# Optimization experiments

Hardware: AMD Instinct MI355X
Metric: run time of the kernel (lower is better)

Reference implementation:

```python
import jax, jax.numpy as jnp
import numpy as np

# Directional rectangle cumulative max: max over the axis-aligned rectangle
# between each pixel and one image corner.

def _rectmax(x, rev_h, rev_w):
    y = jax.lax.cummax(x, axis=2, reverse=rev_h)
    return jax.lax.cummax(y, axis=3, reverse=rev_w)


def _guided_pool(xq, gq, rev_h, rev_w):
    # Guided landmark pool: each pixel takes max of itself and the directional
    # cumulative max restricted to guide==1 positions. With guide == ones this
    # reduces to the plain directional rectangle cummax (the un-guided pool).
    neg = jnp.finfo(xq.dtype).min
    masked = jnp.where(gq > 0, xq, neg)
    return jnp.maximum(xq, _rectmax(masked, rev_h, rev_w))

# (rev_h, rev_w) for TopLeft, TopRight, BottomLeft, BottomRight pools
_DIRS = [(True, True), (True, False), (False, True), (False, False)]


def setup_inputs() -> dict:
    key = jax.random.key(0)
    k1, k2, k3 = jax.random.split(key, 3)
    B, C, H, W = 16, 256, 64, 64
    Cout, K = 256, 3
    x = jax.random.normal(k1, (B, C, H, W), jnp.float32)
    weight = jax.random.normal(k2, (Cout, C, K, K), jnp.float32) * 0.02
    bias = jax.random.normal(k3, (Cout,), jnp.float32) * 0.02
    return {"x": x, "weight": weight, "bias": bias}


def reference(x, weight, bias):
    B, C, H, W = x.shape
    Q = C // 4
    # Original torch code squares x IN PLACE via chunk() views before pooling.
    xsq = x * x
    # Per-quadrant channel energy and its global (row, col) argmax -> one-hot guide.
    energy = xsq.reshape(B, 4, Q, H, W).sum(axis=2)            # [B,4,H,W]
    idx = jnp.argmax(energy.reshape(B, 4, H * W), axis=-1)     # [B,4]
    onehot = (jnp.arange(H * W) == idx[..., None]).astype(x.dtype)
    guide = jnp.broadcast_to(onehot.reshape(B, 4, 1, H, W), (B, 4, Q, H, W)).reshape(B, C, H, W)
    # Four directional guided pools, one per channel quadrant, then conv.
    xs = jnp.split(xsq, 4, axis=1)
    gs = jnp.split(guide, 4, axis=1)
    pooled = jnp.concatenate(
        [_guided_pool(xs[i], gs[i], *_DIRS[i]) for i in range(4)], axis=1)
    out = jax.lax.conv_general_dilated(
        pooled, weight, window_strides=(1, 1), padding='SAME',
        dimension_numbers=('NCHW', 'OIHW', 'NCHW'))
    return out + bias[None, :, None, None]
```

## Files before the change

### kernel.cpp

```cpp
#include <hip/hip_runtime.h>
#include <cstddef>

#define B_   16
#define C_   256
#define HW_  4096

typedef __attribute__((ext_vector_type(8)))  short bf16x8;
typedef __attribute__((ext_vector_type(16))) float f32x16;

static __device__ __forceinline__ unsigned short f2bf(float f) {
    unsigned int u = __float_as_uint(f);
    u += 0x7fffu + ((u >> 16) & 1u);
    return (unsigned short)(u >> 16);
}

__global__ __launch_bounds__(256) void fused_energy(const float* __restrict__ x,
                                                    unsigned short* __restrict__ xsqN,
                                                    float* __restrict__ pval,
                                                    int* __restrict__ pidx) {
    int blk = blockIdx.x;
    int b = blk >> 6, h = blk & 63;
    int tid = threadIdx.x;
    int tl  = tid >> 4;
    int w4  = (tid & 15) << 2;
    int wv  = tid >> 6;
    __shared__ float earr[4][4][64];
    __shared__ unsigned short tile[64][264];
    const float* xb = x + (size_t)b * C_ * HW_ + h * 64 + w4;

    float e[4][4];
#pragma unroll
    for (int q = 0; q < 4; ++q)
#pragma unroll
        for (int ww = 0; ww < 4; ++ww) e[q][ww] = 0.f;

#pragma unroll
    for (int i = 0; i < 4; ++i) {
        int c4 = tl * 4 + 64 * i;
        float sq[4][4];
#pragma unroll
        for (int k = 0; k < 4; ++k) {
            float4 v = *(const float4*)(xb + (size_t)(c4 + k) * HW_);
            sq[k][0] = v.x * v.x; sq[k][1] = v.y * v.y;
            sq[k][2] = v.z * v.z; sq[k][3] = v.w * v.w;
            e[i][0] += sq[k][0]; e[i][1] += sq[k][1];
            e[i][2] += sq[k][2]; e[i][3] += sq[k][3];
        }
#pragma unroll
        for (int ww = 0; ww < 4; ++ww) {
            uint2 p;
            p.x = (unsigned)f2bf(sq[0][ww]) | ((unsigned)f2bf(sq[1][ww]) << 16);
            p.y = (unsigned)f2bf(sq[2][ww]) | ((unsigned)f2bf(sq[3][ww]) << 16);
            *(uint2*)(&tile[w4 + ww][c4]) = p;
        }
    }

#pragma unroll
    for (int q = 0; q < 4; ++q)
#pragma unroll
        for (int ww = 0; ww < 4; ++ww) {
            float v = e[q][ww];
            v += __shfl_xor(v, 16);
            v += __shfl_xor(v, 32);
            e[q][ww] = v;
        }
    if ((tid & 48) == 0) {
#pragma unroll
        for (int q = 0; q < 4; ++q) {
            float4 v; v.x = e[q][0]; v.y = e[q][1]; v.z = e[q][2]; v.w = e[q][3];
            *(float4*)&earr[wv][q][w4] = v;
        }
    }
    __syncthreads();

    size_t base = (size_t)(b * 64 + h) * 64 * 256;
#pragma unroll
    for (int it = 0; it < 8; ++it) {
        int row  = it * 8 + (tid >> 5);
        int col8 = (tid & 31) * 8;
        *(int4*)(xsqN + base + (size_t)row * 256 + col8) = *(int4*)&tile[row][col8];
    }

    int q = tid >> 6;
    int w = tid & 63;
    float ev = earr[0][q][w] + earr[1][q][w] + earr[2][q][w] + earr[3][q][w];
    int ix = h * 64 + w;
#pragma unroll
    for (int off = 32; off; off >>= 1) {
        float ov = __shfl_down(ev, off);
        int   oi = __shfl_down(ix, off);
        if (ov > ev || (ov == ev && oi < ix)) { ev = ov; ix = oi; }
    }
    if ((tid & 63) == 0) {
        pval[(b * 64 + h) * 4 + q] = ev;
        pidx[(b * 64 + h) * 4 + q] = ix;
    }
}

__global__ __launch_bounds__(64) void energy_final(const float* __restrict__ pval,
                                                   const int* __restrict__ pidx,
                                                   int* __restrict__ lm,
                                                   const unsigned short* __restrict__ xsqN,
                                                   unsigned short* __restrict__ Lval) {
    int bq = blockIdx.x;
    int b = bq >> 2, q = bq & 3;
    int t = threadIdx.x;
    float ev = pval[(b * 64 + t) * 4 + q];
    int   ix = pidx[(b * 64 + t) * 4 + q];
#pragma unroll
    for (int off = 32; off; off >>= 1) {
        float ov = __shfl_down(ev, off);
        int   oi = __shfl_down(ix, off);
        if (ov > ev || (ov == ev && oi < ix)) { ev = ov; ix = oi; }
    }
    int ix0 = __shfl(ix, 0);
    if (t == 0) lm[bq] = ix0;
    Lval[b * 256 + q * 64 + t] =
        xsqN[((size_t)((b * 64 + (ix0 >> 6)) * 64 + (ix0 & 63))) * 256 + q * 64 + t];
}

__global__ __launch_bounds__(256) void wt_pack(const float* __restrict__ w,
                                               unsigned short* __restrict__ wa) {
    int blk = blockIdx.x;
    int cog = blk >> 3, cib = blk & 7;
    int tid = threadIdx.x;
    __shared__ unsigned short wlds[32][292];
    {
        int co_l = tid >> 3;
        int seg  = tid & 7;
        const float* src = w + ((size_t)((cog * 32 + co_l) * 256 + cib * 32)) * 9 + seg * 36;
#pragma unroll
        for (int f4 = 0; f4 < 9; ++f4) {
            float4 v = *(const float4*)(src + f4 * 4);
            uint2 p;
            p.x = (unsigned)f2bf(v.x) | ((unsigned)f2bf(v.y) << 16);
            p.y = (unsigned)f2bf(v.z) | ((unsigned)f2bf(v.w) << 16);
            *(uint2*)(&wlds[co_l][seg * 36 + f4 * 4]) = p;
        }
    }
    __syncthreads();
    for (int idx = tid; idx < 1152; idx += 256) {
        int lane = idx & 63;
        int s    = (idx >> 6) & 1;
        int j    = idx >> 7;
        int co_l = lane & 31;
        int k0   = s * 16 + (lane >> 5) * 8;
        union { unsigned short us[8]; int4 v; } u;
#pragma unroll
        for (int jj = 0; jj < 8; ++jj)
            u.us[jj] = wlds[co_l][(k0 + jj) * 9 + j];
        int ob = (cib * 9 + j) * 16 + s * 8 + cog;
        *(int4*)(wa + ((size_t)ob * 64 + lane) * 8) = u.v;
    }
}

static __device__ __forceinline__ void load_B(int4 sv[4],
                                              const unsigned short* __restrict__ xsqN,
                                              int b, int h0, int nc, int tid) {
#pragma unroll
    for (int t2 = 0; t2 < 4; ++t2) {
        int idx = tid + t2 * 512;
        int4 v = {0, 0, 0, 0};
        if (idx < 1584) {
            int pr = idx / 264; int rem = idx - pr * 264;
            int pc = rem >> 2;  int part = rem & 3;
            int grow = h0 - 1 + pr, gcol = pc - 1;
            if ((unsigned)grow < 64u && (unsigned)gcol < 64u)
                v = *(const int4*)(xsqN + (((size_t)(b * 64 + grow) * 64 + gcol) * 256 + nc * 32 + part * 8));
        }
        sv[t2] = v;
    }
}

static __device__ __forceinline__ void store_B(const int4 sv[4],
                                               unsigned short* __restrict__ Bw,
                                               const unsigned short* __restrict__ Lval,
                                               const int* __restrict__ lm,
                                               int b, int h0, int nc, int tid) {
    int l = lm[b * 4 + (nc >> 1)];
    int hm = l >> 6, wm = l & 63;
    bool qhle = (nc >> 1) < 2;
    bool qwle = ((nc >> 1) & 1) == 0;
#pragma unroll
    for (int t2 = 0; t2 < 4; ++t2) {
        int idx = tid + t2 * 512;
        if (idx < 1584) {
            int pr = idx / 264; int rem = idx - pr * 264;
            int pc = rem >> 2;  int part = rem & 3;
            int grow = h0 - 1 + pr, gcol = pc - 1;
            union { int4 v; unsigned short us[8]; } u; u.v = sv[t2];
            bool inb = ((unsigned)grow < 64u) && ((unsigned)gcol < 64u);
            bool hok = qhle ? (grow <= hm) : (grow >= hm);
            bool wok = qwle ? (gcol <= wm) : (gcol >= wm);
            if (inb && hok && wok) {
                union { int4 v; unsigned short us[8]; } Lu;
                Lu.v = *(const int4*)(Lval + b * 256 + nc * 32 + part * 8);
#pragma unroll
                for (int k = 0; k < 8; ++k)
                    if (Lu.us[k] > u.us[k]) u.us[k] = Lu.us[k];
            }
            *(int4*)(&Bw[(pr * 66 + pc) * 40 + part * 8]) = u.v;
        }
    }
}

__global__ __launch_bounds__(512, 2) void conv_mfma(const unsigned short* __restrict__ xsqN,
                                                    const unsigned short* __restrict__ wa,
                                                    const float* __restrict__ bias,
                                                    const int* __restrict__ lm,
                                                    const unsigned short* __restrict__ Lval,
                                                    float* __restrict__ out) {
    int pt = blockIdx.x;
    int b  = pt >> 4;
    int h0 = (pt & 15) * 4;
    int tid  = threadIdx.x;
    int lane = tid & 63;
    int wv   = tid >> 6;
    int wy = wv >> 2, wx = wv & 3;
    int l31 = lane & 31, qh = lane >> 5;

    __shared__ unsigned short Bs[2][6 * 66 * 40];
    __shared__ unsigned short As[2][3 * 8192];

    f32x16 acc[4][2];
#pragma unroll
    for (int mt = 0; mt < 4; ++mt)
#pragma unroll
        for (int nt = 0; nt < 2; ++nt)
#pragma unroll
            for (int r = 0; r < 16; ++r) acc[mt][nt][r] = 0.f;

    int4 sv[4];

    load_B(sv, xsqN, b, h0, 0, tid);
    {
        const unsigned short* s0 = wa + wv * 3072 + lane * 8;
#pragma unroll
        for (int k = 0; k < 6; ++k)
            __builtin_amdgcn_global_load_lds(s0 + k * 512, &As[0][wv * 3072 + k * 512], 16, 0, 0);
    }
    store_B(sv, &Bs[0][0], Lval, lm, b, h0, 0, tid);
    __syncthreads();

    for (int cib = 0; cib < 8; ++cib) {
#pragma unroll
        for (int sub = 0; sub < 3; ++sub) {
            int ph = cib * 3 + sub;

            if (ph < 23) {
                const unsigned short* s0 = wa + (size_t)(ph + 1) * 24576 + wv * 3072 + lane * 8;
                unsigned short* d0 = &As[(ph + 1) & 1][wv * 3072];
#pragma unroll
                for (int k = 0; k < 6; ++k)
                    __builtin_amdgcn_global_load_lds(s0 + k * 512, d0 + k * 512, 16, 0, 0);
            }
            if (sub == 0 && cib < 7)
                load_B(sv, xsqN, b, h0, cib + 1, tid);

            const unsigned short* Ab = &As[ph & 1][0];
            const unsigned short* Bb = &Bs[cib & 1][0];
#pragma unroll
            for (int tt = 0; tt < 3; ++tt) {
                int j  = sub * 3 + tt;
                int r  = wx + j / 3;
                int w0 = l31 + j % 3;
                const unsigned short* Bp = Bb + (r * 66 + w0) * 40 + qh * 8;
                const unsigned short* At = Ab + tt * 8192;
#pragma unroll
                for (int s = 0; s < 2; ++s) {
                    const bf16x8* ap = (const bf16x8*)(At + (((s * 8 + wy * 4) * 64 + lane) << 3));
                    bf16x8 a0 = ap[0];
                    bf16x8 a1 = ap[64];
                    bf16x8 a2 = ap[128];
                    bf16x8 a3 = ap[192];
                    bf16x8 b0 = *(const bf16x8*)(Bp + s * 16);
                    bf16x8 b1 = *(const bf16x8*)(Bp + 1280 + s * 16);
                    acc[0][0] = __builtin_amdgcn_mfma_f32_32x32x16_bf16(a0, b0, acc[0][0], 0, 0, 0);
                    acc[0][1] = __builtin_amdgcn_mfma_f32_32x32x16_bf16(a0, b1, acc[0][1], 0, 0, 0);
                    acc[1][0] = __builtin_amdgcn_mfma_f32_32x32x16_bf16(a1, b0, acc[1][0], 0, 0, 0);
                    acc[1][1] = __builtin_amdgcn_mfma_f32_32x32x16_bf16(a1, b1, acc[1][1], 0, 0, 0);
                    acc[2][0] = __builtin_amdgcn_mfma_f32_32x32x16_bf16(a2, b0, acc[2][0], 0, 0, 0);
                    acc[2][1] = __builtin_amdgcn_mfma_f32_32x32x16_bf16(a2, b1, acc[2][1], 0, 0, 0);
                    acc[3][0] = __builtin_amdgcn_mfma_f32_32x32x16_bf16(a3, b0, acc[3][0], 0, 0, 0);
                    acc[3][1] = __builtin_amdgcn_mfma_f32_32x32x16_bf16(a3, b1, acc[3][1], 0, 0, 0);
                }
            }

            if (sub == 2 && cib < 7)
                store_B(sv, &Bs[(cib + 1) & 1][0], Lval, lm, b, h0, cib + 1, tid);

            __syncthreads();
        }
    }

    int h = h0 + wx;
#pragma unroll
    for (int mt = 0; mt < 4; ++mt) {
#pragma unroll
        for (int nt = 0; nt < 2; ++nt) {
#pragma unroll
            for (int r = 0; r < 16; ++r) {
                int row = (r & 3) + 8 * (r >> 2) + 4 * qh;
                int co  = wy * 128 + mt * 32 + row;
                int w   = nt * 32 + l31;
                out[(((size_t)(b * 256 + co)) * 64 + h) * 64 + w] = acc[mt][nt][r] + bias[co];
            }
        }
    }
}

extern "C" void kernel_launch(void* const* d_in, const int* in_sizes, int n_in,
                              void* d_out, int out_size, void* d_ws, size_t ws_size,
                              hipStream_t stream) {
    const float* x      = (const float*)d_in[0];
    const float* weight = (const float*)d_in[1];
    const float* bias   = (const float*)d_in[2];
    float* out = (float*)d_out;

    char* ws = (char*)d_ws;
    int*            lmp  = (int*)ws;
    float*          pval = (float*)(ws + 256);
    int*            pidx = (int*)(ws + 256 + 16384);
    unsigned short* Lval = (unsigned short*)(ws + 256 + 32768);
    unsigned short* Wa   = (unsigned short*)(ws + 49152);
    unsigned short* xsqN = (unsigned short*)(ws + 49152 + 1179648);

    hipLaunchKernelGGL(fused_energy, dim3(1024), dim3(256), 0, stream, x, xsqN, pval, pidx);
    hipLaunchKernelGGL(energy_final, dim3(64), dim3(64), 0, stream, pval, pidx, lmp, xsqN, Lval);
    hipLaunchKernelGGL(wt_pack, dim3(64), dim3(256), 0, stream, weight, Wa);
    hipLaunchKernelGGL(conv_mfma, dim3(256), dim3(512), 0, stream, xsqN, Wa, bias, lmp, Lval, out);
}
```

Measured before the change: 189.5 us.

## Software-pipeline A fragment loads in conv MFMA loop and defer B global loads

Restructures the inner MFMA loop so each A-fragment pair is prefetched into a double-buffered register set one m-tile ahead. It also reorders the loop to process both k-halves per m-tile, so only two A vectors are live at a time. The next-channel-block B tile's global load now happens just before its LDS store, which removes the int4 staging registers kept live across the whole loop. This lowers register pressure and overlaps LDS reads with MFMAs, but the B global-load latency is no longer hidden behind compute.

```diff
diff --git a/kernel.cpp b/kernel.cpp
--- a/kernel.cpp
+++ b/kernel.cpp
@@ -230,16 +230,15 @@
 #pragma unroll
             for (int r = 0; r < 16; ++r) acc[mt][nt][r] = 0.f;
 
-    int4 sv[4];
-
-    load_B(sv, xsqN, b, h0, 0, tid);
     {
+        int4 sv[4];
+        load_B(sv, xsqN, b, h0, 0, tid);
         const unsigned short* s0 = wa + wv * 3072 + lane * 8;
 #pragma unroll
         for (int k = 0; k < 6; ++k)
             __builtin_amdgcn_global_load_lds(s0 + k * 512, &As[0][wv * 3072 + k * 512], 16, 0, 0);
-    }
-    store_B(sv, &Bs[0][0], Lval, lm, b, h0, 0, tid);
+        store_B(sv, &Bs[0][0], Lval, lm, b, h0, 0, tid);
+    }
     __syncthreads();
 
     for (int cib = 0; cib < 8; ++cib) {
@@ -254,40 +253,53 @@
                 for (int k = 0; k < 6; ++k)
                     __builtin_amdgcn_global_load_lds(s0 + k * 512, d0 + k * 512, 16, 0, 0);
             }
-            if (sub == 0 && cib < 7)
-                load_B(sv, xsqN, b, h0, cib + 1, tid);
 
             const unsigned short* Ab = &As[ph & 1][0];
             const unsigned short* Bb = &Bs[cib & 1][0];
+
+            bf16x8 bf[2][2];
+            bf16x8 aa[2][2];
+
+            {
+                const bf16x8* ap = (const bf16x8*)(Ab + (((wy * 4 + 0) * 64 + lane) << 3));
+                aa[0][0] = ap[0];
+                aa[0][1] = ap[512];
+            }
+
 #pragma unroll
             for (int tt = 0; tt < 3; ++tt) {
                 int j  = sub * 3 + tt;
                 int r  = wx + j / 3;
                 int w0 = l31 + j % 3;
                 const unsigned short* Bp = Bb + (r * 66 + w0) * 40 + qh * 8;
-                const unsigned short* At = Ab + tt * 8192;
-#pragma unroll
-                for (int s = 0; s < 2; ++s) {
-                    const bf16x8* ap = (const bf16x8*)(At + (((s * 8 + wy * 4) * 64 + lane) << 3));
-                    bf16x8 a0 = ap[0];
-                    bf16x8 a1 = ap[64];
-                    bf16x8 a2 = ap[128];
-                    bf16x8 a3 = ap[192];
-                    bf16x8 b0 = *(const bf16x8*)(Bp + s * 16);
-                    bf16x8 b1 = *(const bf16x8*)(Bp + 1280 + s * 16);
-                    acc[0][0] = __builtin_amdgcn_mfma_f32_32x32x16_bf16(a0, b0, acc[0][0], 0, 0, 0);
-                    acc[0][1] = __builtin_amdgcn_mfma_f32_32x32x16_bf16(a0, b1, acc[0][1], 0, 0, 0);
-                    acc[1][0] = __builtin_amdgcn_mfma_f32_32x32x16_bf16(a1, b0, acc[1][0], 0, 0, 0);
-                    acc[1][1] = __builtin_amdgcn_mfma_f32_32x32x16_bf16(a1, b1, acc[1][1], 0, 0, 0);
-                    acc[2][0] = __builtin_amdgcn_mfma_f32_32x32x16_bf16(a2, b0, acc[2][0], 0, 0, 0);
-                    acc[2][1] = __builtin_amdgcn_mfma_f32_32x32x16_bf16(a2, b1, acc[2][1], 0, 0, 0);
-                    acc[3][0] = __builtin_amdgcn_mfma_f32_32x32x16_bf16(a3, b0, acc[3][0], 0, 0, 0);
-                    acc[3][1] = __builtin_amdgcn_mfma_f32_32x32x16_bf16(a3, b1, acc[3][1], 0, 0, 0);
+                bf[0][0] = *(const bf16x8*)(Bp);
+                bf[0][1] = *(const bf16x8*)(Bp + 16);
+                bf[1][0] = *(const bf16x8*)(Bp + 1280);
+                bf[1][1] = *(const bf16x8*)(Bp + 1296);
+#pragma unroll
+                for (int m = 0; m < 4; ++m) {
+                    const int p = m & 1;
+                    if (m < 3) {
+                        const bf16x8* ap = (const bf16x8*)(Ab + tt * 8192 + (((wy * 4 + m + 1) * 64 + lane) << 3));
+                        aa[p ^ 1][0] = ap[0];
+                        aa[p ^ 1][1] = ap[512];
+                    } else if (tt < 2) {
+                        const bf16x8* ap = (const bf16x8*)(Ab + (tt + 1) * 8192 + (((wy * 4 + 0) * 64 + lane) << 3));
+                        aa[p ^ 1][0] = ap[0];
+                        aa[p ^ 1][1] = ap[512];
+                    }
+                    acc[m][0] = __builtin_amdgcn_mfma_f32_32x32x16_bf16(aa[p][0], bf[0][0], acc[m][0], 0, 0, 0);
+                    acc[m][1] = __builtin_amdgcn_mfma_f32_32x32x16_bf16(aa[p][0], bf[1][0], acc[m][1], 0, 0, 0);
+                    acc[m][0] = __builtin_amdgcn_mfma_f32_32x32x16_bf16(aa[p][1], bf[0][1], acc[m][0], 0, 0, 0);
+                    acc[m][1] = __builtin_amdgcn_mfma_f32_32x32x16_bf16(aa[p][1], bf[1][1], acc[m][1], 0, 0, 0);
                 }
             }
 
-            if (sub == 2 && cib < 7)
+            if (sub == 2 && cib < 7) {
+                int4 sv[4];
+                load_B(sv, xsqN, b, h0, cib + 1, tid);
                 store_B(sv, &Bs[(cib + 1) & 1][0], Lval, lm, b, h0, cib + 1, tid);
+            }
 
             __syncthreads();
         }
```

After: 187.2 us. Within noise of the previous version (-1.2%).
